# Performance work log

Measured on AMD Instinct MI355X. Metric: run time of the kernel, lower is better.

The kernel has to match this reference:

```python
import jax, jax.numpy as jnp
import numpy as np

EMBED_DIM = 1024
NUM_HEADS = 16
HEAD_DIM = EMBED_DIM // NUM_HEADS


def setup_inputs() -> dict:
    key = jax.random.key(0)
    ks = jax.random.split(key, 7)
    B, S, E = 2, 2048, EMBED_DIM
    # xavier_uniform bound for square [E, E] weight
    bound = float(np.sqrt(6.0 / (E + E)))
    mkw = lambda k: jax.random.uniform(k, (E, E), jnp.float32, -bound, bound)
    return {
        "query": jax.random.normal(ks[0], (B, S, E), jnp.float32),
        "key": jax.random.normal(ks[1], (B, S, E), jnp.float32),
        "value": jax.random.normal(ks[2], (B, S, E), jnp.float32),
        "Wq": mkw(ks[3]),
        "Wk": mkw(ks[4]),
        "Wv": mkw(ks[5]),
        "Wo": mkw(ks[6]),
    }


def reference(query, key, value, Wq, Wk, Wv, Wo):
    # Chunked sigmoid attention: since sigmoid has no cross-key normalization
    # and all projections are bias-free linear maps, summing per-KV-chunk
    # partial outputs is mathematically identical to the full computation:
    #   out = (sigmoid(scale * Q K^T) @ V) @ Wo^T
    B, L, E = query.shape
    H, D = NUM_HEADS, HEAD_DIM
    scale = D ** -0.5
    q = (query @ Wq.T).reshape(B, L, H, D) * scale   # [B,L,H,D]
    k = (key @ Wk.T).reshape(B, -1, H, D)            # [B,S,H,D]
    v = (value @ Wv.T).reshape(B, -1, H, D)          # [B,S,H,D]
    scores = jax.nn.sigmoid(jnp.einsum('blhd,bshd->bhls', q, k))  # [B,H,L,S]
    o = jnp.einsum('bhls,bshd->blhd', scores, v).reshape(B, L, E)
    return o @ Wo.T
```

## Files before the change

kernel.cpp:

```cpp
#include <hip/hip_runtime.h>

typedef float f32x4 __attribute__((ext_vector_type(4)));
typedef float f32x16 __attribute__((ext_vector_type(16)));
typedef __bf16 bf16x4 __attribute__((ext_vector_type(4)));
typedef __bf16 bf16x8 __attribute__((ext_vector_type(8)));

constexpr int E = 1024;
constexpr int S = 2048;
constexpr int Bsz = 2;
constexpr int H = 16;
constexpr int Dh = 64;
constexpr int M = Bsz * S;
constexpr int E2 = 2048;

#define GLOAD_LDS16(g, l)                                                                 \
  __builtin_amdgcn_global_load_lds((const __attribute__((address_space(1))) void*)(g),    \
                                   (__attribute__((address_space(3))) void*)(l), 16, 0, 0)

__device__ __forceinline__ unsigned pk2(float a, float b) {
  union { __bf16 h[2]; unsigned u; } r;
  r.h[0] = (__bf16)a; r.h[1] = (__bf16)b;
  return r.u;
}

__global__ __launch_bounds__(256) void convert_bf16(
    const float* __restrict__ q, const float* __restrict__ k,
    const float* __restrict__ v, const float* __restrict__ wq,
    const float* __restrict__ wk, const float* __restrict__ wv,
    const float* __restrict__ wo, __bf16* __restrict__ aq,
    __bf16* __restrict__ ak, __bf16* __restrict__ av,
    __bf16* __restrict__ wqkv, __bf16* __restrict__ wob) {
  const int id = blockIdx.y;
  const float* src;
  __bf16* dst;
  int n;
  float scale = 1.0f;
  switch (id) {
    case 0: src = q;  dst = aq;             n = M * E; break;
    case 1: src = k;  dst = ak;             n = M * E; break;
    case 2: src = v;  dst = av;             n = M * E; break;
    case 3: src = wq; dst = wqkv;           n = E * E; scale = -0.18033688f; break;
    case 4: src = wk; dst = wqkv + E * E;   n = E * E; break;
    case 5: src = wv; dst = wqkv + 2 * E * E; n = E * E; break;
    default: src = wo; dst = wob;           n = E * E; break;
  }
  const int stride = gridDim.x * 256 * 8;
  for (int i = (blockIdx.x * 256 + threadIdx.x) * 8; i < n; i += stride) {
    f32x4 a = *reinterpret_cast<const f32x4*>(&src[i]);
    f32x4 b = *reinterpret_cast<const f32x4*>(&src[i + 4]);
    bf16x8 o;
    o[0] = (__bf16)(a[0] * scale); o[1] = (__bf16)(a[1] * scale);
    o[2] = (__bf16)(a[2] * scale); o[3] = (__bf16)(a[3] * scale);
    o[4] = (__bf16)(b[0] * scale); o[5] = (__bf16)(b[1] * scale);
    o[6] = (__bf16)(b[2] * scale); o[7] = (__bf16)(b[3] * scale);
    *reinterpret_cast<bf16x8*>(&dst[i]) = o;
  }
}

template <int TM, int MODE, int KS>
__global__ __launch_bounds__(256) void gemm_bf16nt(
    const __bf16* __restrict__ A0, const __bf16* __restrict__ A1,
    const __bf16* __restrict__ A2, const __bf16* __restrict__ Bw,
    void* __restrict__ C0, void* __restrict__ C1, void* __restrict__ C2) {
  static_assert(TM == 64, "vmcnt literal assumes TM=64 (6 chunks/wave)");
  constexpr int MI  = TM / 32;
  constexpr int NT  = KS / 64;
  constexpr int ACH = TM / 8;
  constexpr int NCH = ACH + 16;
  constexpr int NTN = (MODE == 0) ? 24 : 8;
  constexpr int NWG = NTN * (M / TM);
  constexpr int CPX = NWG / 8;

  __shared__ char smem[2][NCH * 1024];

  const int t    = threadIdx.x;
  const int lane = t & 63;
  const int wid  = t >> 6;
  const int wr   = (wid >> 1) * (TM / 2);
  const int wc   = (wid & 1) * 64;
  const int r16  = lane & 15;

  const int bid = blockIdx.x;
  const int fid = (bid & 7) * CPX + (bid >> 3);
  const int mt  = fid / NTN;
  const int nt  = fid % NTN;
  const int tm  = mt * TM;
  const int tn  = nt * 128;
  const int which = tn >> 10;

  const __bf16* Ab = (MODE == 0) ? (which == 0 ? A0 : which == 1 ? A1 : A2) : A0;

  auto stage = [&](int kt, int buf) {
    const int k0  = kt * 64;
    const int k0b = k0 & 1023;
    char* dst = smem[buf];
#pragma unroll
    for (int c = wid; c < NCH; c += 4) {
      const bool isA = c < ACH;
      const int cc   = isA ? c : c - ACH;
      const int L    = cc * 1024 + lane * 16;
      const int row  = L >> 7;
      const int sw   = ((L >> 4) & 7) ^ (row & 7);
      const __bf16* src = isA ? &Ab[(size_t)(tm + row) * KS + k0 + sw * 8]
                              : &Bw[(size_t)(tn + row) * 1024 + k0b + sw * 8];
      GLOAD_LDS16(src, dst + c * 1024);
    }
  };

  stage(0, 0);
  stage(1, 1);

  f32x4 acc[MI][4] = {};

  for (int kt = 0; kt < NT; ++kt) {
    const int buf = kt & 1;
    if (kt + 1 < NT) {
      asm volatile("s_waitcnt vmcnt(6)" ::: "memory");
    } else {
      asm volatile("s_waitcnt vmcnt(0)" ::: "memory");
    }
    __builtin_amdgcn_s_barrier();
    __builtin_amdgcn_sched_barrier(0);

    const __bf16* As = (const __bf16*)smem[buf];
    const __bf16* Bs = (const __bf16*)(smem[buf] + ACH * 1024);

#pragma unroll
    for (int kc = 0; kc < 2; ++kc) {
      bf16x8 af[MI], bfv[4];
#pragma unroll
      for (int mi = 0; mi < MI; ++mi) {
        int row = wr + mi * 16 + r16;
        int g   = (kc * 4 + (lane >> 4)) ^ (row & 7);
        af[mi] = *reinterpret_cast<const bf16x8*>(&As[row * 64 + g * 8]);
      }
#pragma unroll
      for (int ni = 0; ni < 4; ++ni) {
        int row = wc + ni * 16 + r16;
        int g   = (kc * 4 + (lane >> 4)) ^ (row & 7);
        bfv[ni] = *reinterpret_cast<const bf16x8*>(&Bs[row * 64 + g * 8]);
      }
      __builtin_amdgcn_s_setprio(1);
#pragma unroll
      for (int mi = 0; mi < MI; ++mi)
#pragma unroll
        for (int ni = 0; ni < 4; ++ni)
          acc[mi][ni] = __builtin_amdgcn_mfma_f32_16x16x32_bf16(af[mi], bfv[ni],
                                                                acc[mi][ni], 0, 0, 0);
      __builtin_amdgcn_s_setprio(0);
    }

    __builtin_amdgcn_sched_barrier(0);
    __builtin_amdgcn_s_barrier();
    if (kt + 2 < NT) stage(kt + 2, buf);
  }

#pragma unroll
  for (int mi = 0; mi < MI; ++mi) {
#pragma unroll
    for (int ni = 0; ni < 4; ++ni) {
#pragma unroll
      for (int j = 0; j < 4; ++j) {
        float v = acc[mi][ni][j];
        int m = tm + wr + mi * 16 + ((lane >> 4) << 2) + j;
        int n = tn + wc + ni * 16 + r16;
        if constexpr (MODE == 0) {
          int nl = n & 1023;
          int b = m >> 11, s = m & 2047, h = nl >> 6, d = nl & 63;
          __bf16* Cout = which == 0 ? (__bf16*)C0 : which == 1 ? (__bf16*)C1
                                                              : (__bf16*)C2;
          if (which < 2) {
            Cout[((size_t)(b * H + h) * S + s) * Dh + d] = (__bf16)v;
          } else {
            int ssw = (s & ~12) | ((s & 4) << 1) | ((s & 8) >> 1);
            Cout[((size_t)(b * H + h) * Dh + d) * S + ssw] = (__bf16)v;
          }
        } else {
          ((float*)C0)[(size_t)m * E + n] = v;
        }
      }
    }
  }
}

__global__ __launch_bounds__(64, 2) void attn_sigmoid(const __bf16* __restrict__ Q,
                                                      const __bf16* __restrict__ K,
                                                      const __bf16* __restrict__ Vt,
                                                      __bf16* __restrict__ O) {
  __shared__ char smem[16384];

  const int t    = threadIdx.x;
  const int lane = t & 63;
  const int l31  = lane & 31;
  const int hh   = lane >> 5;
  const int qt   = blockIdx.x >> 1;
  const int ss   = blockIdx.x & 1;
  const int q0   = qt * 64;
  const int h    = blockIdx.y;
  const int b    = blockIdx.z;

  const __bf16* Qh = Q + (size_t)(b * H + h) * S * Dh;
  const __bf16* Kh = K + (size_t)(b * H + h) * S * Dh;
  const __bf16* Vh = Vt + (size_t)(b * H + h) * Dh * S;

  const __bf16* kSrc = Kh + (size_t)(ss * 1024 + (lane >> 3)) * Dh +
                       (((lane & 7) ^ (lane >> 3)) * 8);
  const __bf16* vSrc = Vh + (size_t)(lane >> 2) * S + ss * 1024 +
                       (((lane & 3) ^ ((lane >> 3) & 3)) * 8);

  auto stage = [&](int it, int buf) {
    char* dst = smem + buf * 8192;
#pragma unroll
    for (int j = 0; j < 4; ++j)
      GLOAD_LDS16(kSrc + it * 2048 + j * 512, dst + j * 1024);
#pragma unroll
    for (int j = 0; j < 4; ++j)
      GLOAD_LDS16(vSrc + it * 32 + (size_t)j * 16 * S, dst + 4096 + j * 1024);
  };

  bf16x8 Qf[2][4];
#pragma unroll
  for (int g = 0; g < 2; ++g)
#pragma unroll
    for (int kc = 0; kc < 4; ++kc)
      Qf[g][kc] = *reinterpret_cast<const bf16x8*>(
          &Qh[(size_t)(q0 + g * 32 + l31) * Dh + kc * 16 + hh * 8]);

  stage(0, 0);
  stage(1, 1);

  f32x16 ot[2][2] = {};

#pragma unroll 2
  for (int it = 0; it < 32; ++it) {
    const int buf = it & 1;
    if (it + 1 < 32) {
      asm volatile("s_waitcnt vmcnt(8)" ::: "memory");
    } else {
      asm volatile("s_waitcnt vmcnt(0)" ::: "memory");
    }
    __builtin_amdgcn_sched_barrier(0);

    const __bf16* Kb = (const __bf16*)(smem + buf * 8192);
    const __bf16* Vb = (const __bf16*)(smem + buf * 8192 + 4096);

    bf16x8 kf[4], vf[4];
#pragma unroll
    for (int kc = 0; kc < 4; ++kc) {
      int x = (2 * kc + hh) ^ (l31 & 7);
      kf[kc] = *reinterpret_cast<const bf16x8*>(&Kb[l31 * 64 + x * 8]);
    }
#pragma unroll
    for (int kc2 = 0; kc2 < 2; ++kc2)
#pragma unroll
      for (int dblk = 0; dblk < 2; ++dblk) {
        int row = dblk * 32 + l31;
        int x   = (2 * kc2 + hh) ^ ((l31 >> 1) & 3);
        vf[kc2 * 2 + dblk] = *reinterpret_cast<const bf16x8*>(&Vb[row * 32 + x * 8]);
      }
    asm volatile("s_waitcnt lgkmcnt(0)" ::: "memory");
    __builtin_amdgcn_sched_barrier(0);

    if (it + 2 < 32) stage(it + 2, buf);

    f32x16 s0 = {}, s1 = {};
    __builtin_amdgcn_s_setprio(1);
#pragma unroll
    for (int kc = 0; kc < 4; ++kc) {
      s0 = __builtin_amdgcn_mfma_f32_32x32x16_bf16(kf[kc], Qf[0][kc], s0, 0, 0, 0);
      s1 = __builtin_amdgcn_mfma_f32_32x32x16_bf16(kf[kc], Qf[1][kc], s1, 0, 0, 0);
    }
    __builtin_amdgcn_s_setprio(0);

    bf16x8 F[2][2];
#pragma unroll
    for (int g = 0; g < 2; ++g) {
      union { unsigned u[4]; bf16x8 v; } fu[2];
#pragma unroll
      for (int kc2 = 0; kc2 < 2; ++kc2) {
#pragma unroll
        for (int jj = 0; jj < 4; ++jj) {
          float ya = g ? s1[kc2 * 8 + 2 * jj] : s0[kc2 * 8 + 2 * jj];
          float yb = g ? s1[kc2 * 8 + 2 * jj + 1] : s0[kc2 * 8 + 2 * jj + 1];
          float pa = __builtin_amdgcn_rcpf(1.0f + __builtin_amdgcn_exp2f(ya));
          float pb = __builtin_amdgcn_rcpf(1.0f + __builtin_amdgcn_exp2f(yb));
          fu[kc2].u[jj] = pk2(pa, pb);
        }
        F[g][kc2] = fu[kc2].v;
      }
    }

    __builtin_amdgcn_s_setprio(1);
#pragma unroll
    for (int kc2 = 0; kc2 < 2; ++kc2) {
#pragma unroll
      for (int dblk = 0; dblk < 2; ++dblk) {
        ot[0][dblk] = __builtin_amdgcn_mfma_f32_32x32x16_bf16(
            vf[kc2 * 2 + dblk], F[0][kc2], ot[0][dblk], 0, 0, 0);
        ot[1][dblk] = __builtin_amdgcn_mfma_f32_32x32x16_bf16(
            vf[kc2 * 2 + dblk], F[1][kc2], ot[1][dblk], 0, 0, 0);
      }
    }
    __builtin_amdgcn_s_setprio(0);
  }

  __syncthreads();
  __bf16* Os = (__bf16*)smem;
#pragma unroll
  for (int g = 0; g < 2; ++g) {
    int row = g * 32 + l31;
#pragma unroll
    for (int dblk = 0; dblk < 2; ++dblk)
#pragma unroll
      for (int rp = 0; rp < 4; ++rp) {
        int r  = rp * 4;
        int gg = dblk * 4 + rp;
        int by = row * 128 + ((gg ^ (row & 7)) * 16) + hh * 8;
        float a0 = ot[g][dblk][r];
        float a1 = ot[g][dblk][r + 1];
        float a2 = ot[g][dblk][r + 2];
        float a3 = ot[g][dblk][r + 3];
        unsigned long long val =
            (unsigned long long)pk2(a0, a1) | ((unsigned long long)pk2(a2, a3) << 32);
        *reinterpret_cast<unsigned long long*>((char*)Os + by) = val;
      }
  }
  __syncthreads();
#pragma unroll
  for (int i = 0; i < 8; ++i) {
    int c   = i * 64 + t;
    int row = c >> 3;
    int ch  = c & 7;
    bf16x8 v = *reinterpret_cast<const bf16x8*>(
        (char*)Os + row * 128 + ((ch ^ (row & 7)) * 16));
    *reinterpret_cast<bf16x8*>(
        &O[((size_t)(b * S) + q0 + row) * E2 + ss * 1024 + h * Dh + ch * 8]) = v;
  }
}

extern "C" void kernel_launch(void* const* d_in, const int* in_sizes, int n_in,
                              void* d_out, int out_size, void* d_ws, size_t ws_size,
                              hipStream_t stream) {
  const float* query = (const float*)d_in[0];
  const float* key_  = (const float*)d_in[1];
  const float* value = (const float*)d_in[2];
  const float* Wq    = (const float*)d_in[3];
  const float* Wk    = (const float*)d_in[4];
  const float* Wv    = (const float*)d_in[5];
  const float* Wo    = (const float*)d_in[6];

  char* ws = (char*)d_ws;
  __bf16* aq   = (__bf16*)(ws);
  __bf16* ak   = (__bf16*)(ws + ((size_t)8 << 20));
  __bf16* av   = (__bf16*)(ws + ((size_t)16 << 20));
  __bf16* wqkv = (__bf16*)(ws + ((size_t)24 << 20));
  __bf16* wob  = (__bf16*)(ws + ((size_t)30 << 20));
  __bf16* pq   = (__bf16*)(ws + ((size_t)32 << 20));
  __bf16* pk   = (__bf16*)(ws + ((size_t)40 << 20));
  __bf16* pvt  = (__bf16*)(ws + ((size_t)48 << 20));
  __bf16* ob   = (__bf16*)(ws);

  convert_bf16<<<dim3(512, 7), 256, 0, stream>>>(query, key_, value, Wq, Wk, Wv,
                                                 Wo, aq, ak, av, wqkv, wob);

  gemm_bf16nt<64, 0, 1024><<<1536, 256, 0, stream>>>(
      aq, ak, av, wqkv, pq, pk, pvt);

  attn_sigmoid<<<dim3(S / 32, H, Bsz), 64, 0, stream>>>(pq, pk, pvt, ob);

  gemm_bf16nt<64, 2, 2048><<<512, 256, 0, stream>>>(
      ob, nullptr, nullptr, wob, (float*)d_out, nullptr, nullptr);
}
```

Measured before the change: 142.7 us.

## Add dedicated 128x128-tile QKV projection GEMM with K=32 double-buffered stages

Replaces the templated 64-row QKV projection GEMM with a dedicated kernel using 128x128 output tiles, where each wave computes a 64x64 sub-tile as 4x4 MFMA 16x16x32 fragments. K is staged in 32-wide double-buffered slices with an XOR swizzle. The aim is more operand reuse per LDS load and half as many workgroups, which cuts global and LDS traffic per FLOP. The trade-off is more accumulator registers, possibly lower occupancy, and more barriers per unit of K since each stage is shorter.

```diff
diff --git a/kernel.cpp b/kernel.cpp
--- a/kernel.cpp
+++ b/kernel.cpp
@@ -57,6 +57,119 @@
   }
 }
 
+__global__ __launch_bounds__(256) void gemm_qkv(
+    const __bf16* __restrict__ A0, const __bf16* __restrict__ A1,
+    const __bf16* __restrict__ A2, const __bf16* __restrict__ Bw,
+    __bf16* __restrict__ C0, __bf16* __restrict__ C1, __bf16* __restrict__ C2) {
+  constexpr int NT  = 32;
+  constexpr int NTN = 24;
+  constexpr int NWG = 32 * NTN;
+  constexpr int CPX = NWG / 8;
+
+  __shared__ char smem[2][16384];
+
+  const int t    = threadIdx.x;
+  const int lane = t & 63;
+  const int wid  = t >> 6;
+  const int wr   = (wid >> 1) * 64;
+  const int wc   = (wid & 1) * 64;
+  const int r16  = lane & 15;
+  const int g4   = lane >> 4;
+
+  const int bid = blockIdx.x;
+  const int fid = (bid & 7) * CPX + (bid >> 3);
+  const int mt  = fid / NTN;
+  const int nt  = fid % NTN;
+  const int tm  = mt * 128;
+  const int tn  = nt * 128;
+  const int which = tn >> 10;
+
+  const __bf16* Ab = which == 0 ? A0 : which == 1 ? A1 : A2;
+
+  auto stage = [&](int kt, int buf) {
+    const int k0 = kt * 32;
+    char* dst = smem[buf];
+#pragma unroll
+    for (int c = wid; c < 16; c += 4) {
+      const bool isA = c < 8;
+      const int cc   = isA ? c : c - 8;
+      const int row  = cc * 16 + (lane >> 2);
+      const int sx   = (lane & 3) ^ ((row >> 1) & 3);
+      const __bf16* src = isA ? &Ab[(size_t)(tm + row) * 1024 + k0 + sx * 8]
+                              : &Bw[(size_t)(tn + row) * 1024 + k0 + sx * 8];
+      GLOAD_LDS16(src, dst + c * 1024);
+    }
+  };
+
+  stage(0, 0);
+  stage(1, 1);
+
+  f32x4 acc[4][4] = {};
+
+  for (int kt = 0; kt < NT; ++kt) {
+    const int buf = kt & 1;
+    if (kt + 1 < NT) {
+      asm volatile("s_waitcnt vmcnt(4)" ::: "memory");
+    } else {
+      asm volatile("s_waitcnt vmcnt(0)" ::: "memory");
+    }
+    __builtin_amdgcn_s_barrier();
+    __builtin_amdgcn_sched_barrier(0);
+
+    const char* As = smem[buf];
+    const char* Bs = smem[buf] + 8192;
+
+    bf16x8 af[4], bfv[4];
+#pragma unroll
+    for (int mi = 0; mi < 4; ++mi) {
+      int row = wr + mi * 16 + r16;
+      int g   = g4 ^ ((row >> 1) & 3);
+      af[mi] = *reinterpret_cast<const bf16x8*>(As + row * 64 + g * 16);
+    }
+#pragma unroll
+    for (int ni = 0; ni < 4; ++ni) {
+      int row = wc + ni * 16 + r16;
+      int g   = g4 ^ ((row >> 1) & 3);
+      bfv[ni] = *reinterpret_cast<const bf16x8*>(Bs + row * 64 + g * 16);
+    }
+
+    __builtin_amdgcn_s_setprio(1);
+#pragma unroll
+    for (int mi = 0; mi < 4; ++mi)
+#pragma unroll
+      for (int ni = 0; ni < 4; ++ni)
+        acc[mi][ni] = __builtin_amdgcn_mfma_f32_16x16x32_bf16(af[mi], bfv[ni],
+                                                              acc[mi][ni], 0, 0, 0);
+    __builtin_amdgcn_s_setprio(0);
+
+    __builtin_amdgcn_sched_barrier(0);
+    __builtin_amdgcn_s_barrier();
+    if (kt + 2 < NT) stage(kt + 2, buf);
+  }
+
+#pragma unroll
+  for (int mi = 0; mi < 4; ++mi) {
+#pragma unroll
+    for (int ni = 0; ni < 4; ++ni) {
+#pragma unroll
+      for (int j = 0; j < 4; ++j) {
+        float v = acc[mi][ni][j];
+        int m = tm + wr + mi * 16 + ((lane >> 4) << 2) + j;
+        int n = tn + wc + ni * 16 + r16;
+        int nl = n & 1023;
+        int b = m >> 11, s = m & 2047, h = nl >> 6, d = nl & 63;
+        __bf16* Cout = which == 0 ? C0 : which == 1 ? C1 : C2;
+        if (which < 2) {
+          Cout[((size_t)(b * H + h) * S + s) * Dh + d] = (__bf16)v;
+        } else {
+          int ssw = (s & ~12) | ((s & 4) << 1) | ((s & 8) >> 1);
+          Cout[((size_t)(b * H + h) * Dh + d) * S + ssw] = (__bf16)v;
+        }
+      }
+    }
+  }
+}
+
 template <int TM, int MODE, int KS>
 __global__ __launch_bounds__(256) void gemm_bf16nt(
     const __bf16* __restrict__ A0, const __bf16* __restrict__ A1,
@@ -67,7 +180,7 @@
   constexpr int NT  = KS / 64;
   constexpr int ACH = TM / 8;
   constexpr int NCH = ACH + 16;
-  constexpr int NTN = (MODE == 0) ? 24 : 8;
+  constexpr int NTN = 8;
   constexpr int NWG = NTN * (M / TM);
   constexpr int CPX = NWG / 8;
 
@@ -86,9 +199,8 @@
   const int nt  = fid % NTN;
   const int tm  = mt * TM;
   const int tn  = nt * 128;
-  const int which = tn >> 10;
-
-  const __bf16* Ab = (MODE == 0) ? (which == 0 ? A0 : which == 1 ? A1 : A2) : A0;
+
+  const __bf16* Ab = A0;
 
   auto stage = [&](int kt, int buf) {
     const int k0  = kt * 64;
@@ -164,20 +276,7 @@
         float v = acc[mi][ni][j];
         int m = tm + wr + mi * 16 + ((lane >> 4) << 2) + j;
         int n = tn + wc + ni * 16 + r16;
-        if constexpr (MODE == 0) {
-          int nl = n & 1023;
-          int b = m >> 11, s = m & 2047, h = nl >> 6, d = nl & 63;
-          __bf16* Cout = which == 0 ? (__bf16*)C0 : which == 1 ? (__bf16*)C1
-                                                              : (__bf16*)C2;
-          if (which < 2) {
-            Cout[((size_t)(b * H + h) * S + s) * Dh + d] = (__bf16)v;
-          } else {
-            int ssw = (s & ~12) | ((s & 4) << 1) | ((s & 8) >> 1);
-            Cout[((size_t)(b * H + h) * Dh + d) * S + ssw] = (__bf16)v;
-          }
-        } else {
-          ((float*)C0)[(size_t)m * E + n] = v;
-        }
+        ((float*)C0)[(size_t)m * E + n] = v;
       }
     }
   }
@@ -363,8 +462,7 @@
   convert_bf16<<<dim3(512, 7), 256, 0, stream>>>(query, key_, value, Wq, Wk, Wv,
                                                  Wo, aq, ak, av, wqkv, wob);
 
-  gemm_bf16nt<64, 0, 1024><<<1536, 256, 0, stream>>>(
-      aq, ak, av, wqkv, pq, pk, pvt);
+  gemm_qkv<<<768, 256, 0, stream>>>(aq, ak, av, wqkv, pq, pk, pvt);
 
   attn_sigmoid<<<dim3(S / 32, H, Bsz), 64, 0, stream>>>(pq, pk, pvt, ob);
 
```

New measurement: 135.6 us. 1.05x faster.
